# Kernel optimization log

Hardware: AMD Instinct MI355X
Metric: run time of the kernel (lower is better)

Reference implementation:

```python
import jax, jax.numpy as jnp
import numpy as np

N, D = 131072, 512

def setup_inputs() -> dict:
    key = jax.random.key(0)
    k1, k2, k3 = jax.random.split(key, 3)
    feature = jax.random.normal(k1, (N, D), dtype=jnp.float32)
    mean = jax.random.normal(k2, (D,), dtype=jnp.float32)
    inverse_cov = jax.random.normal(k3, (D, D), dtype=jnp.float32)
    return {"feature": feature, "mean": mean, "inverse_cov": inverse_cov}

def reference(feature, mean, inverse_cov):
    # zero_f: [N, D]
    zero_f = feature - mean
    # diag(zero_f @ inv_cov @ zero_f.T) == rowwise quadratic form,
    # computed without the NxN intermediate: (zero_f @ inv_cov * zero_f).sum(-1)
    quad = jnp.einsum('nd,de,ne->n', zero_f, inverse_cov, zero_f)
    return jnp.mean(quad)
```

## Files before the change

### kernel.cpp

```cpp
#include <hip/hip_runtime.h>
#include <hip/hip_bf16.h>
#include <stdint.h>


typedef __attribute__((ext_vector_type(8))) short short8;
typedef __attribute__((ext_vector_type(4))) float floatx4;

static constexpr int NROWS = 131072;
static constexpr int DDIM  = 512;
static constexpr int BM = 128, BN = 128;
static constexpr int FS_STRIDE = 136;
static constexpr int BS_STRIDE = 40;

__device__ __forceinline__ short f2bf(float f) {
  __bf16 b = (__bf16)f;
  return __builtin_bit_cast(short, b);
}
__device__ __forceinline__ float bf2f(short s) {
  __bf16 b = __builtin_bit_cast(__bf16, s);
  return (float)b;
}

__global__ __launch_bounds__(256) void maha_prep_t(const float* __restrict__ C,
                                                   short* __restrict__ Ct) {
  __shared__ short T[128 * FS_STRIDE];
  const int bt = blockIdx.x;
  const int k0 = (bt & 3) * 128;
  const int e0 = (bt >> 2) * 128;
  const int rr = threadIdx.x >> 5;
  const int cc = threadIdx.x & 31;
#pragma unroll
  for (int p = 0; p < 16; p++) {
    const int k = p * 8 + rr;
    floatx4 v = *(const floatx4*)(C + (size_t)(k0 + k) * DDIM + e0 + cc * 4);
#pragma unroll
    for (int i = 0; i < 4; i++) T[(cc * 4 + i) * FS_STRIDE + k] = f2bf(v[i]);
  }
  __syncthreads();
  const int er = threadIdx.x >> 4;
  const int kc = threadIdx.x & 15;
#pragma unroll
  for (int p = 0; p < 8; p++) {
    const int e = p * 16 + er;
    short8 v = *(const short8*)&T[e * FS_STRIDE + kc * 8];
    *(short8*)(Ct + (size_t)(e0 + e) * DDIM + k0 + kc * 8) = v;
  }
}

__global__ __launch_bounds__(512) void maha_prep_w(const float* __restrict__ C,
                                                   const float* __restrict__ mean,
                                                   float* __restrict__ w,
                                                   float* __restrict__ out) {
  const int e = threadIdx.x;
  float acc = 0.f;
  for (int k = 0; k < DDIM; k += 8) {
#pragma unroll
    for (int i = 0; i < 8; i++)
      acc += mean[k + i] * bf2f(f2bf(C[(size_t)(k + i) * DDIM + e]));
  }
  w[e] = acc;
  if (e == 0) out[0] = 0.0f;
}

__global__ __launch_bounds__(256, 3) void maha_main(const float* __restrict__ F,
                                                    const float* __restrict__ mean,
                                                    const short* __restrict__ Ct,
                                                    const float* __restrict__ w,
                                                    float* __restrict__ out) {
  __shared__ short Fs[BM * FS_STRIDE];
  __shared__ short Bs[BN * BS_STRIDE];
  __shared__ float red[4];

  const int b = blockIdx.x;
  const int mtile = ((b >> 5) << 3) | (b & 7);
  const int etile = (b >> 3) & 3;
  const int m0 = mtile * BM;
  const int e0 = etile * BN;

  const int t    = threadIdx.x;
  const int lane = t & 63;
  const int wave = t >> 6;
  const int wm = wave >> 1, wn = wave & 1;
  const int l15  = lane & 15;
  const int quad = lane >> 4;

  const int rA = t >> 1;
  const int hA = t & 1;
  const float* Fbase = F  + (size_t)(m0 + rA) * DDIM + hA * 16;
  const short* Cbase = Ct + (size_t)(e0 + rA) * DDIM + hA * 16;

  floatx4 pa[2][4];
  short8  pb[2][2];
  const int chunk_base = (e0 >> 5) + 4;

  auto loadpf = [&](int c, int st) {
    const int ch = (chunk_base + c) & 15;
    const floatx4* fp = (const floatx4*)(Fbase + ch * 32);
    pa[st][0] = fp[0]; pa[st][1] = fp[1]; pa[st][2] = fp[2]; pa[st][3] = fp[3];
    const short8* bp = (const short8*)(Cbase + ch * 32);
    pb[st][0] = bp[0]; pb[st][1] = bp[1];
  };

  floatx4 acc[4][4];
#pragma unroll
  for (int i = 0; i < 4; i++)
#pragma unroll
    for (int j = 0; j < 4; j++) acc[i][j] = floatx4{0.f, 0.f, 0.f, 0.f};

  loadpf(0, 0);
  loadpf(1, 1);

#pragma unroll
  for (int c = 0; c < 16; ++c) {
    const int s  = c & 3;
    const int st = c & 1;
    __syncthreads();
    short8 w0, w1;
#pragma unroll
    for (int q = 0; q < 2; q++)
#pragma unroll
      for (int k = 0; k < 4; k++) {
        w0[q * 4 + k] = f2bf(pa[st][q][k]);
        w1[q * 4 + k] = f2bf(pa[st][q + 2][k]);
      }
    *(short8*)&Fs[rA * FS_STRIDE + s * 32 + hA * 16]     = w0;
    *(short8*)&Fs[rA * FS_STRIDE + s * 32 + hA * 16 + 8] = w1;
    *(short8*)&Bs[rA * BS_STRIDE + hA * 16]              = pb[st][0];
    *(short8*)&Bs[rA * BS_STRIDE + hA * 16 + 8]          = pb[st][1];
    if (c < 14) loadpf(c + 2, st);
    __syncthreads();

    short8 af[4], bfv[4];
#pragma unroll
    for (int i = 0; i < 4; i++)
      af[i] = *(const short8*)&Fs[(wm * 64 + i * 16 + l15) * FS_STRIDE + s * 32 + quad * 8];
#pragma unroll
    for (int j = 0; j < 4; j++)
      bfv[j] = *(const short8*)&Bs[(wn * 64 + j * 16 + l15) * BS_STRIDE + quad * 8];
#pragma unroll
    for (int i = 0; i < 4; i++)
#pragma unroll
      for (int j = 0; j < 4; j++)
        acc[i][j] = __builtin_amdgcn_mfma_f32_16x16x32_bf16(af[i], bfv[j], acc[i][j], 0, 0, 0);
  }

  float psum = 0.f;
#pragma unroll
  for (int j = 0; j < 4; j++) {
    const int e_loc = wn * 64 + j * 16 + l15;
    const float wj = w[e0 + e_loc];
    const float mj = mean[e0 + e_loc];
#pragma unroll
    for (int i = 0; i < 4; i++) {
      const int m_base = wm * 64 + i * 16 + quad * 4;
#pragma unroll
      for (int r = 0; r < 4; r++) {
        const float fv = bf2f(Fs[(m_base + r) * FS_STRIDE + e_loc]);
        psum += (acc[i][j][r] - wj) * (fv - mj);
      }
    }
  }

#pragma unroll
  for (int off = 32; off > 0; off >>= 1) psum += __shfl_down(psum, off);
  if (lane == 0) red[wave] = psum;
  __syncthreads();
  if (t == 0) {
    const float tot = (red[0] + red[1] + red[2] + red[3]) * (1.0f / (float)NROWS);
    atomicAdd(out, tot);
  }
}

extern "C" void kernel_launch(void* const* d_in, const int* in_sizes, int n_in,
                              void* d_out, int out_size, void* d_ws, size_t ws_size,
                              hipStream_t stream) {
  const float* feature = (const float*)d_in[0];
  const float* mean    = (const float*)d_in[1];
  const float* invcov  = (const float*)d_in[2];
  float* out = (float*)d_out;

  float* w  = (float*)d_ws;
  short* Ct = (short*)((char*)d_ws + 4096);

  maha_prep_t<<<16, 256, 0, stream>>>(invcov, Ct);
  maha_prep_w<<<1, 512, 0, stream>>>(invcov, mean, w, out);
  maha_main<<<4096, 256, 0, stream>>>(feature, mean, Ct, w, out);
}
```

Baseline: 461.7 us.

## Load MFMA fragments directly from global memory, drop LDS staging and block barriers

The main kernel now gives each block 64 rows and all 512 output columns across 8 waves. Each wave loads its A and B MFMA fragments straight from global memory into registers with double buffering, so the shared-memory tile and the two barriers per k-step are gone. Each wave writes only the bf16 feature slice it needs for the epilogue into a private LDS bounce buffer. The w precompute is parallelised to one block per output column, reading the transposed bf16 matrix. The cost is that every wave reloads the same feature rows from global memory/cache, eight times per block, and the uncoalesced fragment-shaped loads may waste bandwidth.

```diff
diff --git a/kernel.cpp b/kernel.cpp
--- a/kernel.cpp
+++ b/kernel.cpp
@@ -8,9 +8,8 @@
 
 static constexpr int NROWS = 131072;
 static constexpr int DDIM  = 512;
-static constexpr int BM = 128, BN = 128;
 static constexpr int FS_STRIDE = 136;
-static constexpr int BS_STRIDE = 40;
+static constexpr int BSTRIDE = 72;
 
 __device__ __forceinline__ short f2bf(float f) {
   __bf16 b = (__bf16)f;
@@ -47,58 +46,59 @@
   }
 }
 
-__global__ __launch_bounds__(512) void maha_prep_w(const float* __restrict__ C,
-                                                   const float* __restrict__ mean,
-                                                   float* __restrict__ w,
-                                                   float* __restrict__ out) {
-  const int e = threadIdx.x;
-  float acc = 0.f;
-  for (int k = 0; k < DDIM; k += 8) {
+__global__ __launch_bounds__(64) void maha_prep_w(const short* __restrict__ Ct,
+                                                  const float* __restrict__ mean,
+                                                  float* __restrict__ w,
+                                                  float* __restrict__ out) {
+  const int e = blockIdx.x;
+  const int t = threadIdx.x;
+  short8 cv = *(const short8*)(Ct + (size_t)e * DDIM + t * 8);
+  float p = 0.f;
 #pragma unroll
-    for (int i = 0; i < 8; i++)
-      acc += mean[k + i] * bf2f(f2bf(C[(size_t)(k + i) * DDIM + e]));
+  for (int i = 0; i < 8; i++) p += mean[t * 8 + i] * bf2f(cv[i]);
+#pragma unroll
+  for (int off = 32; off > 0; off >>= 1) p += __shfl_down(p, off);
+  if (t == 0) {
+    w[e] = p;
+    if (e == 0) out[0] = 0.0f;
   }
-  w[e] = acc;
-  if (e == 0) out[0] = 0.0f;
 }
 
-__global__ __launch_bounds__(256, 3) void maha_main(const float* __restrict__ F,
+__global__ __launch_bounds__(512, 2) void maha_main(const float* __restrict__ F,
                                                     const float* __restrict__ mean,
                                                     const short* __restrict__ Ct,
                                                     const float* __restrict__ w,
                                                     float* __restrict__ out) {
-  __shared__ short Fs[BM * FS_STRIDE];
-  __shared__ short Bs[BN * BS_STRIDE];
-  __shared__ float red[4];
-
-  const int b = blockIdx.x;
-  const int mtile = ((b >> 5) << 3) | (b & 7);
-  const int etile = (b >> 3) & 3;
-  const int m0 = mtile * BM;
-  const int e0 = etile * BN;
+  __shared__ short bounce[8 * 64 * BSTRIDE];
+  __shared__ float red[8];
 
   const int t    = threadIdx.x;
   const int lane = t & 63;
-  const int wave = t >> 6;
-  const int wm = wave >> 1, wn = wave & 1;
+  const int wv   = t >> 6;
   const int l15  = lane & 15;
   const int quad = lane >> 4;
 
-  const int rA = t >> 1;
-  const int hA = t & 1;
-  const float* Fbase = F  + (size_t)(m0 + rA) * DDIM + hA * 16;
-  const short* Cbase = Ct + (size_t)(e0 + rA) * DDIM + hA * 16;
+  const int m0 = blockIdx.x * 64;
+  const int e0 = wv * 64;
 
-  floatx4 pa[2][4];
-  short8  pb[2][2];
-  const int chunk_base = (e0 >> 5) + 4;
+  const float* Abase = F  + (size_t)(m0 + l15) * DDIM + quad * 8;
+  const short* Bbase = Ct + (size_t)(e0 + l15) * DDIM + quad * 8;
 
-  auto loadpf = [&](int c, int st) {
-    const int ch = (chunk_base + c) & 15;
-    const floatx4* fp = (const floatx4*)(Fbase + ch * 32);
-    pa[st][0] = fp[0]; pa[st][1] = fp[1]; pa[st][2] = fp[2]; pa[st][3] = fp[3];
-    const short8* bp = (const short8*)(Cbase + ch * 32);
-    pb[st][0] = bp[0]; pb[st][1] = bp[1];
+  floatx4 pA[2][8];
+  short8  pB[2][4];
+
+  auto loadA = [&](int ks, int st) {
+#pragma unroll
+    for (int mi = 0; mi < 4; mi++) {
+      const floatx4* p = (const floatx4*)(Abase + mi * 16 * DDIM + ks * 32);
+      pA[st][mi * 2]     = p[0];
+      pA[st][mi * 2 + 1] = p[1];
+    }
+  };
+  auto loadB = [&](int ks, int st) {
+#pragma unroll
+    for (int fj = 0; fj < 4; fj++)
+      pB[st][fj] = *(const short8*)(Bbase + fj * 16 * DDIM + ks * 32);
   };
 
   floatx4 acc[4][4];
@@ -107,67 +107,64 @@
 #pragma unroll
     for (int j = 0; j < 4; j++) acc[i][j] = floatx4{0.f, 0.f, 0.f, 0.f};
 
-  loadpf(0, 0);
-  loadpf(1, 1);
+  loadA(0, 0); loadB(0, 0);
+  loadA(1, 1); loadB(1, 1);
+
+  short* myb = bounce + wv * 64 * BSTRIDE;
 
 #pragma unroll
   for (int c = 0; c < 16; ++c) {
-    const int s  = c & 3;
     const int st = c & 1;
-    __syncthreads();
-    short8 w0, w1;
+    short8 af[4];
 #pragma unroll
-    for (int q = 0; q < 2; q++)
+    for (int mi = 0; mi < 4; mi++)
 #pragma unroll
-      for (int k = 0; k < 4; k++) {
-        w0[q * 4 + k] = f2bf(pa[st][q][k]);
-        w1[q * 4 + k] = f2bf(pa[st][q + 2][k]);
+      for (int j = 0; j < 4; j++) {
+        af[mi][j]     = f2bf(pA[st][mi * 2][j]);
+        af[mi][j + 4] = f2bf(pA[st][mi * 2 + 1][j]);
       }
-    *(short8*)&Fs[rA * FS_STRIDE + s * 32 + hA * 16]     = w0;
-    *(short8*)&Fs[rA * FS_STRIDE + s * 32 + hA * 16 + 8] = w1;
-    *(short8*)&Bs[rA * BS_STRIDE + hA * 16]              = pb[st][0];
-    *(short8*)&Bs[rA * BS_STRIDE + hA * 16 + 8]          = pb[st][1];
-    if (c < 14) loadpf(c + 2, st);
-    __syncthreads();
-
-    short8 af[4], bfv[4];
+    if (c + 2 < 16) loadA(c + 2, st);
+    if ((c >> 1) == wv) {
+      const int half = c & 1;
 #pragma unroll
-    for (int i = 0; i < 4; i++)
-      af[i] = *(const short8*)&Fs[(wm * 64 + i * 16 + l15) * FS_STRIDE + s * 32 + quad * 8];
+      for (int mi = 0; mi < 4; mi++)
+        *(short8*)&myb[(mi * 16 + l15) * BSTRIDE + half * 32 + quad * 8] = af[mi];
+    }
 #pragma unroll
-    for (int j = 0; j < 4; j++)
-      bfv[j] = *(const short8*)&Bs[(wn * 64 + j * 16 + l15) * BS_STRIDE + quad * 8];
+    for (int fj = 0; fj < 4; fj++)
 #pragma unroll
-    for (int i = 0; i < 4; i++)
-#pragma unroll
-      for (int j = 0; j < 4; j++)
-        acc[i][j] = __builtin_amdgcn_mfma_f32_16x16x32_bf16(af[i], bfv[j], acc[i][j], 0, 0, 0);
+      for (int mi = 0; mi < 4; mi++)
+        acc[mi][fj] = __builtin_amdgcn_mfma_f32_16x16x32_bf16(af[mi], pB[st][fj],
+                                                              acc[mi][fj], 0, 0, 0);
+    if (c + 2 < 16) loadB(c + 2, st);
   }
 
   float psum = 0.f;
 #pragma unroll
-  for (int j = 0; j < 4; j++) {
-    const int e_loc = wn * 64 + j * 16 + l15;
+  for (int fj = 0; fj < 4; fj++) {
+    const int e_loc = fj * 16 + l15;
     const float wj = w[e0 + e_loc];
     const float mj = mean[e0 + e_loc];
 #pragma unroll
-    for (int i = 0; i < 4; i++) {
-      const int m_base = wm * 64 + i * 16 + quad * 4;
+    for (int mi = 0; mi < 4; mi++) {
+      const int rbase = mi * 16 + quad * 4;
 #pragma unroll
       for (int r = 0; r < 4; r++) {
-        const float fv = bf2f(Fs[(m_base + r) * FS_STRIDE + e_loc]);
-        psum += (acc[i][j][r] - wj) * (fv - mj);
+        const float fv = bf2f(myb[(rbase + r) * BSTRIDE + e_loc]);
+        psum += (acc[mi][fj][r] - wj) * (fv - mj);
       }
     }
   }
 
 #pragma unroll
   for (int off = 32; off > 0; off >>= 1) psum += __shfl_down(psum, off);
-  if (lane == 0) red[wave] = psum;
+  if (lane == 0) red[wv] = psum;
   __syncthreads();
   if (t == 0) {
-    const float tot = (red[0] + red[1] + red[2] + red[3]) * (1.0f / (float)NROWS);
-    atomicAdd(out, tot);
+    float tot = 0.f;
+#pragma unroll
+    for (int i = 0; i < 8; i++) tot += red[i];
+    atomicAdd(out, tot * (1.0f / (float)NROWS));
   }
 }
 
@@ -183,6 +180,6 @@
   short* Ct = (short*)((char*)d_ws + 4096);
 
   maha_prep_t<<<16, 256, 0, stream>>>(invcov, Ct);
-  maha_prep_w<<<1, 512, 0, stream>>>(invcov, mean, w, out);
-  maha_main<<<4096, 256, 0, stream>>>(feature, mean, Ct, w, out);
+  maha_prep_w<<<512, 64, 0, stream>>>(Ct, mean, w, out);
+  maha_main<<<2048, 512, 0, stream>>>(feature, mean, Ct, w, out);
 }
```

Result: slower. 642.2 us (+39.1%).
